# Performance work log

Measured on AMD Instinct MI355X. Metric: run time of the kernel, lower is better.

Reference implementation:

```python
import jax, jax.numpy as jnp
import numpy as np

DIM = 1024
B, T = 4, 8192


def setup_inputs() -> dict:
    key = jax.random.key(0)
    ks = jax.random.split(key, 5)
    scale = 1.0 / np.sqrt(DIM)
    x = jax.random.normal(ks[0], (B, T, DIM), dtype=jnp.float32)
    w_in = jax.random.uniform(ks[1], (DIM, DIM), jnp.float32, -scale, scale)
    b_in = jax.random.uniform(ks[2], (DIM,), jnp.float32, -scale, scale)
    a = jnp.zeros((DIM,), jnp.float32)   # nn.Parameter(torch.zeros(dim))
    b = jnp.ones((DIM,), jnp.float32)    # nn.Parameter(torch.ones(dim))
    w_out = jax.random.uniform(ks[3], (DIM, DIM), jnp.float32, -scale, scale)
    b_out = jax.random.uniform(ks[4], (DIM,), jnp.float32, -scale, scale)
    return {"x": x, "w_in": w_in, "b_in": b_in, "a": a, "b": b,
            "w_out": w_out, "b_out": b_out}


def reference(x, w_in, b_in, a, b, w_out, b_out):
    # h = in_proj(x): [B, T, D]
    h = jnp.einsum('btd,ed->bte', x, w_in) + b_in
    A = jax.nn.sigmoid(a)  # [D], diagonal transition

    def step(state, h_t):
        state = A * state + b * h_t  # [B, D]
        return state, state

    init = jnp.zeros_like(h[:, 0])  # [B, D]
    _, ys = jax.lax.scan(step, init, jnp.swapaxes(h, 0, 1))  # ys: [T, B, D]
    y = jnp.swapaxes(ys, 0, 1)  # [B, T, D]
    return jnp.einsum('btd,ed->bte', y, w_out) + b_out
```

## Files before the change

kernel.cpp:

```cpp
#include <hip/hip_runtime.h>
#include <hip/hip_bf16.h>
#include <cstdint>

#define DIM 1024
#define BATCH 4
#define SEQ 8192
#define M_TOTAL (BATCH * SEQ)

#define CH 64
#define CL (SEQ / CH)

using bf16 = __hip_bfloat16;
typedef __attribute__((ext_vector_type(16))) float f32x16;
typedef __attribute__((ext_vector_type(8))) __bf16 bf16x8;

__global__ void convert_all(const float* __restrict__ x, bf16* __restrict__ xb,
                            const float* __restrict__ w1, bf16* __restrict__ w1b,
                            const float* __restrict__ w2, bf16* __restrict__ w2b,
                            long n4x, long n4w) {
    long i = blockIdx.x * (long)blockDim.x + threadIdx.x;
    const float* in;
    bf16* out;
    long off;
    if (i < n4x)              { in = x;  out = xb;  off = i; }
    else if (i < n4x + n4w)   { in = w1; out = w1b; off = i - n4x; }
    else if (i < n4x + 2*n4w) { in = w2; out = w2b; off = i - n4x - n4w; }
    else return;
    const float4 v = ((const float4*)in)[off];
    __hip_bfloat162* o = (__hip_bfloat162*)(out + off * 4);
    o[0] = __float22bfloat162_rn(make_float2(v.x, v.y));
    o[1] = __float22bfloat162_rn(make_float2(v.z, v.w));
}

template <int OUT_MODE>
__global__ __launch_bounds__(256) void gemm_bt_kernel(
    const bf16* __restrict__ A, const bf16* __restrict__ B,
    const float* __restrict__ bias, void* __restrict__ C,
    int M, int N, int K) {
    __shared__ __align__(16) char lds[2 * 128 * 64 * 2];
    char* ldsA = lds;
    char* ldsB = lds + 128 * 64 * 2;

    const int tid  = threadIdx.x;
    const int wave = tid >> 6;
    const int lane = tid & 63;

    const int L   = blockIdx.x;
    const int xcd = L & 7;
    const int li  = L >> 3;
    const int bm  = xcd * 32 + (li >> 3);
    const int bn  = li & 7;

    const int wm = (wave >> 1) * 64;
    const int wn = (wave & 1) * 64;

    f32x16 acc[2][2];
#pragma unroll
    for (int i = 0; i < 2; i++)
#pragma unroll
        for (int j = 0; j < 2; j++)
#pragma unroll
            for (int r = 0; r < 16; r++) acc[i][j][r] = 0.f;

    const long arow_base = (long)bm * 128;
    const long brow_base = (long)bn * 128;

    const int r31   = lane & 31;
    const int khalf = lane >> 5;

    for (int k0 = 0; k0 < K; k0 += 64) {
#pragma unroll
        for (int r = 0; r < 4; r++) {
            int c = tid + r * 256;
            int row = c >> 3;
            int kc = (c & 7) ^ (row & 7);
            const bf16* ga = A + (arow_base + row) * (long)K + k0 + kc * 8;
            const bf16* gb = B + (brow_base + row) * (long)K + k0 + kc * 8;
            __builtin_amdgcn_global_load_lds(
                (const __attribute__((address_space(1))) void*)ga,
                (__attribute__((address_space(3))) void*)(ldsA + c * 16),
                16, 0, 0);
            __builtin_amdgcn_global_load_lds(
                (const __attribute__((address_space(1))) void*)gb,
                (__attribute__((address_space(3))) void*)(ldsB + c * 16),
                16, 0, 0);
        }
        __syncthreads();

#pragma unroll
        for (int s = 0; s < 4; s++) {
            const int kc = s * 2 + khalf;
            bf16x8 af[2], bfv[2];
#pragma unroll
            for (int i = 0; i < 2; i++) {
                int row = wm + i * 32 + r31;
                int chunk = row * 8 + (kc ^ (row & 7));
                af[i] = *(const bf16x8*)(ldsA + chunk * 16);
            }
#pragma unroll
            for (int j = 0; j < 2; j++) {
                int row = wn + j * 32 + r31;
                int chunk = row * 8 + (kc ^ (row & 7));
                bfv[j] = *(const bf16x8*)(ldsB + chunk * 16);
            }
#pragma unroll
            for (int i = 0; i < 2; i++)
#pragma unroll
                for (int j = 0; j < 2; j++)
                    acc[i][j] = __builtin_amdgcn_mfma_f32_32x32x16_bf16(
                        af[i], bfv[j], acc[i][j], 0, 0, 0);
        }
        __syncthreads();
    }

    const int ccol  = lane & 31;
    const int rbase = 4 * (lane >> 5);
#pragma unroll
    for (int i = 0; i < 2; i++) {
#pragma unroll
        for (int j = 0; j < 2; j++) {
            int n = bn * 128 + wn + j * 32 + ccol;
            float bv = bias[n];
#pragma unroll
            for (int r = 0; r < 16; r++) {
                int rowt = (r & 3) + 8 * (r >> 2) + rbase;
                long m = (long)bm * 128 + wm + i * 32 + rowt;
                float v = acc[i][j][r] + bv;
                long idx = m * (long)N + n;
                if (OUT_MODE == 0)
                    ((bf16*)C)[idx] = __float2bfloat16(v);
                else
                    ((float*)C)[idx] = v;
            }
        }
    }
}

__global__ __launch_bounds__(512) void scan_pass1(
    const bf16* __restrict__ h, const float* __restrict__ a,
    const float* __restrict__ bcoef, float* __restrict__ S) {
    const int d2 = threadIdx.x;
    const int blk = blockIdx.x;
    const int b = blk / CH, c = blk % CH;
    const float A0 = 1.f / (1.f + expf(-a[2 * d2]));
    const float A1 = 1.f / (1.f + expf(-a[2 * d2 + 1]));
    const float b0 = bcoef[2 * d2];
    const float b1 = bcoef[2 * d2 + 1];
    float s0 = 0.f, s1 = 0.f;
    const __hip_bfloat162* hp =
        (const __hip_bfloat162*)(h + ((long)b * SEQ + (long)c * CL) * DIM) + d2;
#pragma unroll 8
    for (int t = 0; t < CL; t++) {
        float2 v = __bfloat1622float2(hp[(long)t * (DIM / 2)]);
        s0 = A0 * s0 + b0 * v.x;
        s1 = A1 * s1 + b1 * v.y;
    }
    float2* Sp = (float2*)(S + ((long)b * CH + c) * DIM) + d2;
    *Sp = make_float2(s0, s1);
}

__global__ __launch_bounds__(512) void scan_pass3(
    bf16* __restrict__ h, const float* __restrict__ a,
    const float* __restrict__ bcoef, const float* __restrict__ S) {
    const int d2 = threadIdx.x;
    const int blk = blockIdx.x;
    const int b = blk / CH, c = blk % CH;
    const float A0 = 1.f / (1.f + expf(-a[2 * d2]));
    const float A1 = 1.f / (1.f + expf(-a[2 * d2 + 1]));
    const float b0 = bcoef[2 * d2];
    const float b1 = bcoef[2 * d2 + 1];
    float Ap0 = A0, Ap1 = A1;
#pragma unroll
    for (int i = 0; i < 7; i++) { Ap0 *= Ap0; Ap1 *= Ap1; }

    float c0 = 0.f, c1 = 0.f;
    const float2* Sp = (const float2*)(S + (long)b * CH * DIM) + d2;
    for (int i0 = 0; i0 < c; i0 += 8) {
        float2 sv[8];
        int nn = (c - i0 < 8) ? (c - i0) : 8;
#pragma unroll 8
        for (int j = 0; j < 8; j++)
            if (j < nn) sv[j] = Sp[(long)(i0 + j) * (DIM / 2)];
#pragma unroll 8
        for (int j = 0; j < 8; j++)
            if (j < nn) { c0 = Ap0 * c0 + sv[j].x; c1 = Ap1 * c1 + sv[j].y; }
    }

    float s0 = c0, s1 = c1;
    __hip_bfloat162* hp =
        (__hip_bfloat162*)(h + ((long)b * SEQ + (long)c * CL) * DIM) + d2;
#pragma unroll 8
    for (int t = 0; t < CL; t++) {
        float2 v = __bfloat1622float2(hp[(long)t * (DIM / 2)]);
        s0 = A0 * s0 + b0 * v.x;
        s1 = A1 * s1 + b1 * v.y;
        hp[(long)t * (DIM / 2)] = __float22bfloat162_rn(make_float2(s0, s1));
    }
}

extern "C" void kernel_launch(void* const* d_in, const int* in_sizes, int n_in,
                              void* d_out, int out_size, void* d_ws,
                              size_t ws_size, hipStream_t stream) {
    const float* x     = (const float*)d_in[0];
    const float* w_in  = (const float*)d_in[1];
    const float* b_in  = (const float*)d_in[2];
    const float* a     = (const float*)d_in[3];
    const float* bcoef = (const float*)d_in[4];
    const float* w_out = (const float*)d_in[5];
    const float* b_out = (const float*)d_in[6];
    float* out = (float*)d_out;

    char* ws = (char*)d_ws;
    bf16* xb  = (bf16*)ws;  ws += (size_t)M_TOTAL * DIM * 2;
    bf16* wib = (bf16*)ws;  ws += (size_t)DIM * DIM * 2;
    bf16* wob = (bf16*)ws;  ws += (size_t)DIM * DIM * 2;
    bf16* h   = (bf16*)ws;  ws += (size_t)M_TOTAL * DIM * 2;
    float* S  = (float*)ws; ws += (size_t)BATCH * CH * DIM * 4;

    {
        long n4x = (long)M_TOTAL * DIM / 4;
        long n4w = (long)DIM * DIM / 4;
        long total = n4x + 2 * n4w;
        convert_all<<<(int)((total + 255) / 256), 256, 0, stream>>>(
            x, xb, w_in, wib, w_out, wob, n4x, n4w);
    }

    const int nblocks = (M_TOTAL / 128) * (DIM / 128);

    gemm_bt_kernel<0><<<nblocks, 256, 0, stream>>>(xb, wib, b_in, h,
                                                   M_TOTAL, DIM, DIM);

    scan_pass1<<<BATCH * CH, 512, 0, stream>>>(h, a, bcoef, S);
    scan_pass3<<<BATCH * CH, 512, 0, stream>>>(h, a, bcoef, S);

    gemm_bt_kernel<1><<<nblocks, 256, 0, stream>>>(h, wob, b_out, out,
                                                   M_TOTAL, DIM, DIM);
}
```

Measured before the change: 418.9 us.

## Use pipelined 256x256 MFMA GEMM and fuse chunk scan pass into epilogue

Replaces the 128x128 GEMM with a 256x256-tile, 512-thread kernel that uses 16x16x32 MFMAs and double-buffered LDS staging, interleaving global-to-LDS loads with compute under explicit barriers and waitcnts. The first GEMM's epilogue also writes its bf16 output tile into LDS and computes the per-chunk scan partial sums (the old scan_pass1) directly from it, so h is not re-read from global memory. The tile mapping relies on CL equaling 128 rows per half tile. The design depends on tight hand-written synchronization, and 128KB of LDS per block limits occupancy.

```diff
diff --git a/kernel.cpp b/kernel.cpp
--- a/kernel.cpp
+++ b/kernel.cpp
@@ -11,8 +11,19 @@
 #define CL (SEQ / CH)
 
 using bf16 = __hip_bfloat16;
-typedef __attribute__((ext_vector_type(16))) float f32x16;
+typedef __attribute__((ext_vector_type(4))) float f32x4;
 typedef __attribute__((ext_vector_type(8))) __bf16 bf16x8;
+
+#define NT (DIM / 64)
+#define NI (NT / 2)
+
+#define BAR() asm volatile("s_barrier" ::: "memory")
+#define WAIT_LGKM0()                                    \
+  do {                                                  \
+    asm volatile("s_waitcnt lgkmcnt(0)" ::: "memory");  \
+    __builtin_amdgcn_sched_barrier(0);                  \
+  } while (0)
+#define WAIT_VM(n) asm volatile("s_waitcnt vmcnt(" #n ")" ::: "memory")
 
 __global__ void convert_all(const float* __restrict__ x, bf16* __restrict__ xb,
                             const float* __restrict__ w1, bf16* __restrict__ w1b,
@@ -32,131 +43,194 @@
     o[1] = __float22bfloat162_rn(make_float2(v.z, v.w));
 }
 
+__device__ __forceinline__ void stage_half(const bf16* __restrict__ g,
+                                           char* ldsbase, int tid) {
+    const int w = tid >> 6, l = tid & 63;
+    const int kc = (l & 7) ^ ((l >> 3) & 7);
+#pragma unroll
+    for (int j = 0; j < 2; j++) {
+        const int idx = (w * 2 + j) * 64 + l;
+        const int row = w * 16 + j * 8 + (l >> 3);
+        const bf16* src = g + (size_t)row * DIM + kc * 8;
+        __builtin_amdgcn_global_load_lds(
+            (const __attribute__((address_space(1))) void*)src,
+            (__attribute__((address_space(3))) void*)(ldsbase + idx * 16),
+            16, 0, 0);
+    }
+}
+
 template <int OUT_MODE>
-__global__ __launch_bounds__(256) void gemm_bt_kernel(
+__global__ __launch_bounds__(512, 2) void gemm256(
     const bf16* __restrict__ A, const bf16* __restrict__ B,
     const float* __restrict__ bias, void* __restrict__ C,
-    int M, int N, int K) {
-    __shared__ __align__(16) char lds[2 * 128 * 64 * 2];
-    char* ldsA = lds;
-    char* ldsB = lds + 128 * 64 * 2;
+    const float* __restrict__ acoef, const float* __restrict__ bcoef,
+    float* __restrict__ S) {
+    __shared__ __align__(16) char lds[131072];
 
     const int tid  = threadIdx.x;
     const int wave = tid >> 6;
-    const int lane = tid & 63;
-
-    const int L   = blockIdx.x;
-    const int xcd = L & 7;
-    const int li  = L >> 3;
-    const int bm  = xcd * 32 + (li >> 3);
-    const int bn  = li & 7;
-
-    const int wm = (wave >> 1) * 64;
-    const int wn = (wave & 1) * 64;
-
-    f32x16 acc[2][2];
-#pragma unroll
-    for (int i = 0; i < 2; i++)
-#pragma unroll
-        for (int j = 0; j < 2; j++)
-#pragma unroll
-            for (int r = 0; r < 16; r++) acc[i][j][r] = 0.f;
-
-    const long arow_base = (long)bm * 128;
-    const long brow_base = (long)bn * 128;
-
-    const int r31   = lane & 31;
-    const int khalf = lane >> 5;
-
-    for (int k0 = 0; k0 < K; k0 += 64) {
-#pragma unroll
-        for (int r = 0; r < 4; r++) {
-            int c = tid + r * 256;
-            int row = c >> 3;
-            int kc = (c & 7) ^ (row & 7);
-            const bf16* ga = A + (arow_base + row) * (long)K + k0 + kc * 8;
-            const bf16* gb = B + (brow_base + row) * (long)K + k0 + kc * 8;
-            __builtin_amdgcn_global_load_lds(
-                (const __attribute__((address_space(1))) void*)ga,
-                (__attribute__((address_space(3))) void*)(ldsA + c * 16),
-                16, 0, 0);
-            __builtin_amdgcn_global_load_lds(
-                (const __attribute__((address_space(1))) void*)gb,
-                (__attribute__((address_space(3))) void*)(ldsB + c * 16),
-                16, 0, 0);
+    const int l    = tid & 63;
+
+    const int orig = blockIdx.x;
+    const int xcd  = orig & 7;
+    const int li   = orig >> 3;
+    const int bm   = xcd * 16 + (li >> 2);
+    const int bn   = li & 3;
+
+    const bf16* Abase = A + (size_t)bm * 256 * DIM;
+    const bf16* Bbase = B + (size_t)bn * 256 * DIM;
+
+    char* pa0 = lds + (wave >> 2) * 16384;
+    char* pb0 = lds + 32768 + ((wave & 3) >> 1) * 16384 + (wave & 1) * 8192;
+    char* pa1 = pa0 + 65536;
+    char* pb1 = pb0 + 65536;
+
+    const int rl = l & 15;
+    const int lg = l >> 4;
+    const int r7 = l & 7;
+    const int ao0 = rl * 128 + ((lg ^ r7) << 4);
+    const int ao1 = rl * 128 + (((4 + lg) ^ r7) << 4);
+
+    f32x4 acc[8][4];
+#pragma unroll
+    for (int m = 0; m < 8; m++)
+#pragma unroll
+        for (int n = 0; n < 4; n++)
+#pragma unroll
+            for (int r = 0; r < 4; r++) acc[m][n][r] = 0.f;
+
+    bf16x8 af[4][2], bfr[4][2];
+
+#define READ_A4(PA, FMB)                                                   \
+    _Pragma("unroll") for (int m_ = 0; m_ < 4; m_++) {                     \
+        af[m_][0] = *(const bf16x8*)((PA) + (FMB + m_) * 2048 + ao0);      \
+        af[m_][1] = *(const bf16x8*)((PA) + (FMB + m_) * 2048 + ao1);      \
+    }
+#define READ_B2(PB, FNB)                                                   \
+    _Pragma("unroll") for (int n_ = 0; n_ < 2; n_++) {                     \
+        bfr[FNB + n_][0] = *(const bf16x8*)((PB) + (FNB + n_) * 2048 + ao0); \
+        bfr[FNB + n_][1] = *(const bf16x8*)((PB) + (FNB + n_) * 2048 + ao1); \
+    }
+#define MFMA16(MB, NB2)                                                    \
+    __builtin_amdgcn_s_setprio(1);                                         \
+    _Pragma("unroll") for (int m_ = 0; m_ < 4; m_++)                       \
+    _Pragma("unroll") for (int n_ = 0; n_ < 2; n_++)                       \
+    _Pragma("unroll") for (int k_ = 0; k_ < 2; k_++)                       \
+        acc[MB + m_][NB2 + n_] = __builtin_amdgcn_mfma_f32_16x16x32_bf16(  \
+            af[m_][k_], bfr[NB2 + n_][k_], acc[MB + m_][NB2 + n_], 0, 0, 0); \
+    __builtin_amdgcn_s_setprio(0);
+
+    stage_half(Abase,                          lds +     0, tid);
+    stage_half(Abase + (size_t)128 * DIM,      lds + 16384, tid);
+    stage_half(Bbase,                          lds + 32768, tid);
+    stage_half(Bbase + (size_t)128 * DIM,      lds + 49152, tid);
+    stage_half(Bbase + 64,                     lds + 65536 + 32768, tid);
+    stage_half(Bbase + (size_t)128 * DIM + 64, lds + 65536 + 49152, tid);
+    WAIT_VM(4);
+    BAR();
+
+    for (int i = 0; i < NI; ++i) {
+        const bool last = (i == NI - 1);
+        const size_t kt1 = (size_t)(2 * i + 1) * 64;
+        const size_t kt2 = kt1 + 64;
+        const size_t kt3 = kt1 + 128;
+
+        READ_A4(pa0, 0); READ_B2(pb0, 0);
+        stage_half(Abase + kt1, lds + 65536, tid);
+        BAR(); WAIT_LGKM0(); MFMA16(0, 0); BAR();
+
+        READ_B2(pb0, 2);
+        stage_half(Abase + (size_t)128 * DIM + kt1, lds + 65536 + 16384, tid);
+        BAR(); WAIT_LGKM0(); MFMA16(0, 2); BAR();
+
+        READ_A4(pa0, 4);
+        if (!last) stage_half(Bbase + kt2, lds + 32768, tid);
+        BAR(); WAIT_LGKM0(); MFMA16(4, 0); BAR();
+
+        if (!last)
+            stage_half(Bbase + (size_t)128 * DIM + kt2, lds + 49152, tid);
+        BAR(); WAIT_LGKM0(); MFMA16(4, 2);
+        if (last) { WAIT_VM(0); } else { WAIT_VM(4); }
+        BAR();
+
+        READ_A4(pa1, 0); READ_B2(pb1, 0);
+        if (!last) stage_half(Abase + kt2, lds + 0, tid);
+        BAR(); WAIT_LGKM0(); MFMA16(0, 0); BAR();
+
+        READ_B2(pb1, 2);
+        if (!last) stage_half(Abase + (size_t)128 * DIM + kt2, lds + 16384, tid);
+        BAR(); WAIT_LGKM0(); MFMA16(0, 2); BAR();
+
+        READ_A4(pa1, 4);
+        if (!last) stage_half(Bbase + kt3, lds + 65536 + 32768, tid);
+        BAR(); WAIT_LGKM0(); MFMA16(4, 0); BAR();
+
+        if (!last)
+            stage_half(Bbase + (size_t)128 * DIM + kt3, lds + 65536 + 49152, tid);
+        BAR(); WAIT_LGKM0(); MFMA16(4, 2);
+        if (!last) { WAIT_VM(4); }
+        BAR();
+    }
+
+    const int wm = (wave >> 2) * 128;
+    const int wn = (wave & 3) * 64;
+    const long mb = (long)bm * 256 + wm;
+    const int nb = bn * 256 + wn;
+    const int crow = lg * 4;
+
+    float bv[4];
+#pragma unroll
+    for (int n = 0; n < 4; n++) bv[n] = bias[nb + n * 16 + rl];
+
+    if (OUT_MODE == 1) {
+        float* O = (float*)C;
+#pragma unroll
+        for (int m = 0; m < 8; m++)
+#pragma unroll
+            for (int n = 0; n < 4; n++) {
+                const int col = nb + n * 16 + rl;
+#pragma unroll
+                for (int r = 0; r < 4; r++)
+                    O[(mb + m * 16 + crow + r) * (long)DIM + col] =
+                        acc[m][n][r] + bv[n];
+            }
+    } else {
+        bf16* H = (bf16*)C;
+#pragma unroll
+        for (int m = 0; m < 8; m++)
+#pragma unroll
+            for (int n = 0; n < 4; n++) {
+                const int col  = nb + n * 16 + rl;
+                const int lcol = wn + n * 16 + rl;
+#pragma unroll
+                for (int r = 0; r < 4; r++) {
+                    const int lrow = wm + m * 16 + crow + r;
+                    const bf16 hv = __float2bfloat16(acc[m][n][r] + bv[n]);
+                    H[(mb + m * 16 + crow + r) * (long)DIM + col] = hv;
+                    const int cb = (lcol * 2) ^ (((lrow >> 2) & 7) << 4);
+                    *(bf16*)(lds + lrow * 512 + cb) = hv;
+                }
+            }
+        asm volatile("s_waitcnt lgkmcnt(0)" ::: "memory");
+        BAR();
+        const int c   = tid & 255;
+        const int ch2 = tid >> 8;
+        const int d   = bn * 256 + c;
+        const float Ad = 1.f / (1.f + expf(-acoef[d]));
+        const float bd = bcoef[d];
+        float s = 0.f;
+#pragma unroll 8
+        for (int t = 0; t < CL; t++) {
+            const int lrow = ch2 * 128 + t;
+            const int cb = (c * 2) ^ (((lrow >> 2) & 7) << 4);
+            const float v = __bfloat162float(*(const bf16*)(lds + lrow * 512 + cb));
+            s = Ad * s + bd * v;
         }
-        __syncthreads();
-
-#pragma unroll
-        for (int s = 0; s < 4; s++) {
-            const int kc = s * 2 + khalf;
-            bf16x8 af[2], bfv[2];
-#pragma unroll
-            for (int i = 0; i < 2; i++) {
-                int row = wm + i * 32 + r31;
-                int chunk = row * 8 + (kc ^ (row & 7));
-                af[i] = *(const bf16x8*)(ldsA + chunk * 16);
-            }
-#pragma unroll
-            for (int j = 0; j < 2; j++) {
-                int row = wn + j * 32 + r31;
-                int chunk = row * 8 + (kc ^ (row & 7));
-                bfv[j] = *(const bf16x8*)(ldsB + chunk * 16);
-            }
-#pragma unroll
-            for (int i = 0; i < 2; i++)
-#pragma unroll
-                for (int j = 0; j < 2; j++)
-                    acc[i][j] = __builtin_amdgcn_mfma_f32_32x32x16_bf16(
-                        af[i], bfv[j], acc[i][j], 0, 0, 0);
-        }
-        __syncthreads();
-    }
-
-    const int ccol  = lane & 31;
-    const int rbase = 4 * (lane >> 5);
-#pragma unroll
-    for (int i = 0; i < 2; i++) {
-#pragma unroll
-        for (int j = 0; j < 2; j++) {
-            int n = bn * 128 + wn + j * 32 + ccol;
-            float bv = bias[n];
-#pragma unroll
-            for (int r = 0; r < 16; r++) {
-                int rowt = (r & 3) + 8 * (r >> 2) + rbase;
-                long m = (long)bm * 128 + wm + i * 32 + rowt;
-                float v = acc[i][j][r] + bv;
-                long idx = m * (long)N + n;
-                if (OUT_MODE == 0)
-                    ((bf16*)C)[idx] = __float2bfloat16(v);
-                else
-                    ((float*)C)[idx] = v;
-            }
-        }
-    }
-}
-
-__global__ __launch_bounds__(512) void scan_pass1(
-    const bf16* __restrict__ h, const float* __restrict__ a,
-    const float* __restrict__ bcoef, float* __restrict__ S) {
-    const int d2 = threadIdx.x;
-    const int blk = blockIdx.x;
-    const int b = blk / CH, c = blk % CH;
-    const float A0 = 1.f / (1.f + expf(-a[2 * d2]));
-    const float A1 = 1.f / (1.f + expf(-a[2 * d2 + 1]));
-    const float b0 = bcoef[2 * d2];
-    const float b1 = bcoef[2 * d2 + 1];
-    float s0 = 0.f, s1 = 0.f;
-    const __hip_bfloat162* hp =
-        (const __hip_bfloat162*)(h + ((long)b * SEQ + (long)c * CL) * DIM) + d2;
-#pragma unroll 8
-    for (int t = 0; t < CL; t++) {
-        float2 v = __bfloat1622float2(hp[(long)t * (DIM / 2)]);
-        s0 = A0 * s0 + b0 * v.x;
-        s1 = A1 * s1 + b1 * v.y;
-    }
-    float2* Sp = (float2*)(S + ((long)b * CH + c) * DIM) + d2;
-    *Sp = make_float2(s0, s1);
+        S[((long)bm * 2 + ch2) * DIM + d] = s;
+    }
+#undef READ_A4
+#undef READ_B2
+#undef MFMA16
 }
 
 __global__ __launch_bounds__(512) void scan_pass3(
@@ -225,14 +299,12 @@
             x, xb, w_in, wib, w_out, wob, n4x, n4w);
     }
 
-    const int nblocks = (M_TOTAL / 128) * (DIM / 128);
-
-    gemm_bt_kernel<0><<<nblocks, 256, 0, stream>>>(xb, wib, b_in, h,
-                                                   M_TOTAL, DIM, DIM);
-
-    scan_pass1<<<BATCH * CH, 512, 0, stream>>>(h, a, bcoef, S);
+    const int nblocks = (M_TOTAL / 256) * (DIM / 256);
+
+    gemm256<0><<<nblocks, 512, 0, stream>>>(xb, wib, b_in, h, a, bcoef, S);
+
     scan_pass3<<<BATCH * CH, 512, 0, stream>>>(h, a, bcoef, S);
 
-    gemm_bt_kernel<1><<<nblocks, 256, 0, stream>>>(h, wob, b_out, out,
-                                                   M_TOTAL, DIM, DIM);
-}
+    gemm256<1><<<nblocks, 512, 0, stream>>>(h, wob, b_out, out,
+                                            nullptr, nullptr, nullptr);
+}
```

Result: faster. 390.4 us (-6.8%).
